# Optimization experiments

Hardware: AMD Instinct MI355X
Metric: run time of the kernel (lower is better)

Reference implementation:

```python
import jax, jax.numpy as jnp
import numpy as np

NEG_SLOPE = 0.2  # PyG GATv2 default leaky_relu slope

N_NODES = 50000
N_EDGES = 800000
F_IN = 128
HEADS = 4
C_HID = 32   # hidden_dim per head; concat -> 128
C_EMB = 128  # embedding_dim (concat=False, mean over heads)
OUT_DIM = 2


def _glorot(key, shape):
    fan_in, fan_out = shape[0], shape[-1]
    lim = (6.0 / (fan_in + fan_out)) ** 0.5
    return jax.random.uniform(key, shape, jnp.float32, -lim, lim)


def setup_inputs() -> dict:
    key = jax.random.key(0)
    ks = jax.random.split(key, 12)
    x = jax.random.normal(ks[0], (N_NODES, F_IN), jnp.float32)
    edge_index = jax.random.randint(ks[1], (2, N_EDGES), 0, N_NODES, jnp.int64)
    params = {
        # layer 1: F_IN -> (HEADS, C_HID), concat=True
        "Wl1": _glorot(ks[2], (F_IN, HEADS * C_HID)),
        "Wr1": _glorot(ks[3], (F_IN, HEADS * C_HID)),
        "att1": _glorot(ks[4], (HEADS, C_HID)),
        "b1": jnp.zeros((HEADS * C_HID,), jnp.float32),
        # layer 2: HEADS*C_HID -> (HEADS, C_EMB), concat=False (mean)
        "Wl2": _glorot(ks[5], (HEADS * C_HID, HEADS * C_EMB)),
        "Wr2": _glorot(ks[6], (HEADS * C_HID, HEADS * C_EMB)),
        "att2": _glorot(ks[7], (HEADS, C_EMB)),
        "b2": jnp.zeros((C_EMB,), jnp.float32),
        # decoder linear
        "Wo": _glorot(ks[8], (C_EMB, OUT_DIM)),
        "bo": jnp.zeros((OUT_DIM,), jnp.float32),
    }
    return {"x": x, "edge_index": edge_index, **params}


def _gatv2_layer(x, Wl, Wr, att, b, src, dst, n_nodes, concat):
    """GATv2Conv: e_ij = att . leaky_relu(Wl x_j + Wr x_i); segment softmax over dst."""
    H, C = att.shape
    xl = (x @ Wl).reshape(n_nodes, H, C)  # source transform
    xr = (x @ Wr).reshape(n_nodes, H, C)  # target transform
    m = xl[src] + xr[dst]                                  # [E,H,C]
    e = jnp.sum(jax.nn.leaky_relu(m, NEG_SLOPE) * att, axis=-1)  # [E,H]
    # numerically stable segment softmax over edges sharing a dst node
    emax = jax.ops.segment_max(e, dst, num_segments=n_nodes)[dst]
    ex = jnp.exp(e - emax)
    denom = jax.ops.segment_sum(ex, dst, num_segments=n_nodes)[dst]
    alpha = ex / denom                                     # [E,H]
    out = jax.ops.segment_sum(alpha[..., None] * xl[src], dst, num_segments=n_nodes)  # [N,H,C]
    out = out.reshape(n_nodes, H * C) if concat else out.mean(axis=1)
    return out + b


def reference(x, edge_index, Wl1, Wr1, att1, b1, Wl2, Wr2, att2, b2, Wo, bo):
    n = x.shape[0]
    loop = jnp.arange(n, dtype=edge_index.dtype)
    src = jnp.concatenate([edge_index[0], loop])  # PyG adds self-loops by default
    dst = jnp.concatenate([edge_index[1], loop])
    h = _gatv2_layer(x, Wl1, Wr1, att1, b1, src, dst, n, concat=True)
    h = jax.nn.relu(h)
    h = _gatv2_layer(h, Wl2, Wr2, att2, b2, src, dst, n, concat=False)
    out = h @ Wo + bo
    return out, h
```

## Files before the change

kernel.cpp:

```cpp
#include <hip/hip_runtime.h>

#define NEG_SLOPE 0.2f
#define LOG2E 1.44269504088896340736f

typedef unsigned short ushort_t;
typedef unsigned int uint_t;
typedef __attribute__((ext_vector_type(8))) short bf16x8;
typedef __attribute__((ext_vector_type(4))) float f32x4;
typedef __attribute__((ext_vector_type(2))) float f32x2;

__device__ inline float bf2f(ushort_t u) { union { uint_t i; float f; } v; v.i = ((uint_t)u) << 16; return v.f; }
__device__ inline ushort_t f2bf(float f) {
    union { float f; uint_t u; } v; v.f = f;
    uint_t r = v.u + 0x7fffu + ((v.u >> 16) & 1u);
    return (ushort_t)(r >> 16);
}
__device__ inline f32x2 up2v(uint_t w) {
    union { uint_t i; float f; } lo, hi;
    lo.i = w << 16; hi.i = w & 0xFFFF0000u;
    return (f32x2){lo.f, hi.f};
}
__device__ inline f32x2 up2f(uint_t w) {
    union { uint_t i; float f; } lo, hi;
    lo.i = w << 16; hi.i = w;
    return (f32x2){lo.f, hi.f};
}
__device__ inline float ld_f(const void* p, size_t i, int bf) { return bf ? bf2f(((const ushort_t*)p)[i]) : ((const float*)p)[i]; }
__device__ inline ushort_t ld_b(const void* p, size_t i, int bf) { return bf ? ((const ushort_t*)p)[i] : f2bf(((const float*)p)[i]); }
__device__ inline void edge_sd(const int* __restrict__ ei, int e, int E_in, int i64, int& src, int& dst) {
    if (e < E_in) {
        if (i64) { src = ei[2 * (size_t)e]; dst = ei[2 * ((size_t)E_in + e)]; }
        else     { src = ei[e];             dst = ei[(size_t)E_in + e]; }
    } else { src = dst = e - E_in; }
}

template <int CTRL>
__device__ inline float dpp_add(float v) {
    union { float f; int i; } u, r;
    u.f = v;
    r.i = __builtin_amdgcn_update_dpp(0, u.i, CTRL, 0xF, 0xF, true);
    return v + r.f;
}

__device__ inline uint4 ldu4(const ushort_t* __restrict__ base, uint_t boff) {
    return *(const uint4*)((const char*)base + (size_t)boff);
}

__global__ void k_detect(const uint_t* __restrict__ xw, const int* __restrict__ ei, int* flags) {
    __shared__ int cnt;
    if (threadIdx.x == 0) cnt = 0;
    __syncthreads();
    uint_t w = xw[threadIdx.x];
    int eb = (int)((w >> 7) & 0xFFu);
    if (eb >= 113 && eb <= 142) atomicAdd(&cnt, 1);
    __syncthreads();
    if (threadIdx.x == 0) {
        flags[0] = (cnt > 128) ? 1 : 0;
        int z = 0;
        #pragma unroll
        for (int i = 1; i < 16; i += 2) z += (ei[i] == 0) ? 1 : 0;
        flags[1] = (z == 8) ? 1 : 0;
    }
}

__global__ __launch_bounds__(256) void k_prep(const void* __restrict__ x, const void* Wl1, const void* Wr1,
                      const void* att1, const void* b1, const void* Wl2, const void* Wr2,
                      const void* att2, const void* b2, const void* Wo, const void* bo,
                      const int* __restrict__ ei, int E_in, int Etot, int* deg, ushort_t* xb,
                      ushort_t* WTl1, ushort_t* WTr1, ushort_t* WTl2, ushort_t* WTr2,
                      float* att1f, float* b1f, float* att2f, float* b2f, float* Wof, float* bof,
                      int N, int sW1, int sW2, int satt1, int sb1, int satt2, int sb2, int sWo, int sbo,
                      const int* flags) {
    int bf = flags[0];
    long r = (long)blockIdx.x * 256 + threadIdx.x;
    if (r < Etot) {
        int e = (int)r, dst;
        if (e < E_in) dst = flags[1] ? ei[2 * ((size_t)E_in + e)] : ei[(size_t)E_in + e];
        else          dst = e - E_in;
        atomicAdd(&deg[dst], 1);
        return;
    }
    r -= Etot;
    long nx = (long)N * 128;
    if (r < nx) { xb[r] = ld_b(x, r, bf); return; }          r -= nx;
    if (r < sW1) { int n = r >> 7, k = r & 127; WTl1[r] = ld_b(Wl1, (size_t)k * 128 + n, bf); return; } r -= sW1;
    if (r < sW1) { int n = r >> 7, k = r & 127; WTr1[r] = ld_b(Wr1, (size_t)k * 128 + n, bf); return; } r -= sW1;
    if (r < sW2) { int n = r >> 7, k = r & 127; WTl2[r] = ld_b(Wl2, (size_t)k * 512 + n, bf); return; } r -= sW2;
    if (r < sW2) { int n = r >> 7, k = r & 127; WTr2[r] = ld_b(Wr2, (size_t)k * 512 + n, bf); return; } r -= sW2;
    if (r < satt1) { att1f[r] = ld_f(att1, r, bf); return; } r -= satt1;
    if (r < sb1)   { b1f[r]   = ld_f(b1, r, bf);   return; } r -= sb1;
    if (r < satt2) { att2f[r] = ld_f(att2, r, bf); return; } r -= satt2;
    if (r < sb2)   { b2f[r]   = ld_f(b2, r, bf);   return; } r -= sb2;
    if (r < sWo)   { Wof[r]   = ld_f(Wo, r, bf);   return; } r -= sWo;
    if (r < sbo)   { bof[r]   = ld_f(bo, r, bf);   return; }
}

__global__ __launch_bounds__(256) void k_scanA(const int* __restrict__ deg, int* offs, int* bsum, int n) {
    __shared__ int sh[256];
    int t = threadIdx.x;
    int i = blockIdx.x * 256 + t;
    int v = (i < n) ? deg[i] : 0;
    sh[t] = v; __syncthreads();
    #pragma unroll
    for (int off = 1; off < 256; off <<= 1) {
        int u = (t >= off) ? sh[t - off] : 0;
        __syncthreads();
        sh[t] += u; __syncthreads();
    }
    if (i < n) offs[i] = sh[t] - v;
    if (t == 255) bsum[blockIdx.x] = sh[255];
}

__global__ __launch_bounds__(256) void k_scanBC(int* offs, int* cursor, const int* __restrict__ bsum,
                                                int nb, int n) {
    __shared__ int sh[256];
    int t = threadIdx.x;
    int v = (t < nb) ? bsum[t] : 0;
    sh[t] = v; __syncthreads();
    #pragma unroll
    for (int off = 1; off < 256; off <<= 1) {
        int u = (t >= off) ? sh[t - off] : 0;
        __syncthreads();
        sh[t] += u; __syncthreads();
    }
    if (blockIdx.x == 0 && t == 0) { offs[n] = sh[nb - 1]; cursor[n] = sh[nb - 1]; }
    int base = (blockIdx.x > 0) ? sh[blockIdx.x - 1] : 0;
    __syncthreads();
    int i = blockIdx.x * 256 + t;
    if (i < n) {
        int o = offs[i] + base;
        offs[i] = o; cursor[i] = o;
    }
}

__global__ void k_fill(const int* __restrict__ ei, int E_in, int Etot, const int* flags,
                       int* cursor, int* s_src) {
    int e = blockIdx.x * blockDim.x + threadIdx.x;
    if (e >= Etot) return;
    int src, dst; edge_sd(ei, e, E_in, flags[1], src, dst);
    int p = atomicAdd(&cursor[dst], 1);
    s_src[p] = src;
}

#define BPAD 136
template <int NOUT>
__global__ __launch_bounds__(256) void k_gemm2(const ushort_t* __restrict__ X,
                                               const ushort_t* __restrict__ WTl,
                                               const ushort_t* __restrict__ WTr,
                                               ushort_t* __restrict__ Yl,
                                               ushort_t* __restrict__ Yr, int M) {
    __shared__ ushort_t smem[2 * 64 * BPAD];
    const int lane = threadIdx.x & 63, wid = threadIdx.x >> 6;
    const int rt = blockIdx.x * 4 + wid;
    const bool active = rt < (M >> 4);
    const int quad = lane >> 4, lo = lane & 15;

    bf16x8 afr[4];
    if (active) {
        const ushort_t* xrow = X + (size_t)(rt * 16 + lo) * 128 + quad * 8;
        #pragma unroll
        for (int kc = 0; kc < 4; kc++) afr[kc] = *(const bf16x8*)(xrow + kc * 32);
    }

    for (int g = 0; g < NOUT / 64; g++) {
        __syncthreads();
        #pragma unroll
        for (int i = 0; i < 8; i++) {
            int vecid = threadIdx.x * 8 + i;
            int side = vecid >> 10, row = (vecid >> 4) & 63, v = vecid & 15;
            const ushort_t* src = (side ? WTr : WTl) + (size_t)(g * 64 + row) * 128 + v * 8;
            *(bf16x8*)(smem + (size_t)(side * 64 + row) * BPAD + v * 8) = *(const bf16x8*)src;
        }
        __syncthreads();
        if (!active) continue;
        #pragma unroll
        for (int side = 0; side < 2; side++) {
            ushort_t* Y = side ? Yr : Yl;
            f32x4 acc[4];
            #pragma unroll
            for (int nt = 0; nt < 4; nt++) acc[nt] = (f32x4){0.f, 0.f, 0.f, 0.f};
            #pragma unroll
            for (int nt = 0; nt < 4; nt++) {
                const ushort_t* brow = smem + (size_t)(side * 64 + nt * 16 + lo) * BPAD + quad * 8;
                #pragma unroll
                for (int kc = 0; kc < 4; kc++) {
                    bf16x8 b = *(const bf16x8*)(brow + kc * 32);
                    acc[nt] = __builtin_amdgcn_mfma_f32_16x16x32_bf16(afr[kc], b, acc[nt], 0, 0, 0);
                }
            }
            #pragma unroll
            for (int nt = 0; nt < 4; nt++) {
                int col = g * 64 + nt * 16 + lo;
                #pragma unroll
                for (int ri = 0; ri < 4; ri++) {
                    int row = rt * 16 + quad * 4 + ri;
                    Y[(size_t)row * NOUT + col] = f2bf(acc[nt][ri]);
                }
            }
        }
    }
}

__global__ __launch_bounds__(256) void k_l1(const ushort_t* __restrict__ xl,
                                            const ushort_t* __restrict__ xr,
                                            const int* __restrict__ offs,
                                            const int* __restrict__ s_src,
                                            const float* __restrict__ att,
                                            const float* __restrict__ b1,
                                            int n, ushort_t* __restrict__ h1) {
    int lane = threadIdx.x & 63, wid = threadIdx.x >> 6;
    int node = blockIdx.x * 4 + wid;
    if (node >= n) return;
    int slot = lane >> 4, sub = lane & 15;
    int chb = sub * 8;
    uint_t cb = (uint_t)(sub * 16);

    uint4 xw = *(const uint4*)(xr + (size_t)node * 128 + chb);
    f32x2 xv[4] = {up2v(xw.x), up2v(xw.y), up2v(xw.z), up2v(xw.w)};
    f32x2 aL[4];
    #pragma unroll
    for (int j = 0; j < 4; j++) {
        f32x2 a = {att[chb + 2 * j], att[chb + 2 * j + 1]};
        aL[j] = a * (float)LOG2E;
    }

    int o0 = offs[node], o1 = offs[node + 1];
    float s = 0.f;
    f32x2 acc[4] = {{0.f,0.f},{0.f,0.f},{0.f,0.f},{0.f,0.f}};

    int i = o0 + slot;
    uint_t q0 = 0, q1 = 0;
    uint4 w0 = {0,0,0,0}, w1 = {0,0,0,0};
    if (i < o1)      w0 = ldu4(xl, (((uint_t)s_src[i])      << 8) + cb);
    if (i + 4 < o1)  w1 = ldu4(xl, (((uint_t)s_src[i + 4])  << 8) + cb);
    if (i + 8 < o1)  q0 = (((uint_t)s_src[i + 8])  << 8) + cb;
    if (i + 12 < o1) q1 = (((uint_t)s_src[i + 12]) << 8) + cb;

    while (i < o1) {
        uint4 wc = w0;
        w0 = w1;
        if (i + 8 < o1) w1 = ldu4(xl, q0);
        q0 = q1;
        if (i + 16 < o1) q1 = (((uint_t)s_src[i + 16]) << 8) + cb;
        f32x2 v[4] = {up2v(wc.x), up2v(wc.y), up2v(wc.z), up2v(wc.w)};
        f32x2 es = {0.f, 0.f};
        #pragma unroll
        for (int j = 0; j < 4; j++) {
            f32x2 m = v[j] + xv[j];
            f32x2 l = __builtin_elementwise_max(m, m * NEG_SLOPE);
            es = __builtin_elementwise_fma(aL[j], l, es);
        }
        float e = es.x + es.y;
        e = dpp_add<0xB1>(e);
        e = dpp_add<0x4E>(e);
        float p = __builtin_amdgcn_exp2f(fminf(e, 115.f));
        s += p;
        f32x2 pp = {p, p};
        #pragma unroll
        for (int j = 0; j < 4; j++)
            acc[j] = __builtin_elementwise_fma(pp, v[j], acc[j]);
        i += 4;
    }
    #pragma unroll
    for (int off = 16; off <= 32; off <<= 1) {
        s += __shfl_xor(s, off, 64);
        #pragma unroll
        for (int j = 0; j < 4; j++) {
            f32x2 o = {__shfl_xor(acc[j].x, off, 64), __shfl_xor(acc[j].y, off, 64)};
            acc[j] += o;
        }
    }
    if (slot == 0) {
        float inv = 1.f / s;
        uint_t pk[4];
        #pragma unroll
        for (int j = 0; j < 4; j++) {
            float r0 = fmaxf(fmaf(acc[j].x, inv, b1[chb + 2 * j]),     0.f);
            float r1 = fmaxf(fmaf(acc[j].y, inv, b1[chb + 2 * j + 1]), 0.f);
            pk[j] = (uint_t)f2bf(r0) | ((uint_t)f2bf(r1) << 16);
        }
        *(uint4*)(h1 + (size_t)node * 128 + chb) = make_uint4(pk[0], pk[1], pk[2], pk[3]);
    }
}

__global__ __launch_bounds__(256) void k_l2(const ushort_t* __restrict__ xl,
                                            const ushort_t* __restrict__ xr,
                                            const int* __restrict__ offs,
                                            const int* __restrict__ s_src,
                                            const float* __restrict__ att,
                                            const float* __restrict__ b2,
                                            const float* __restrict__ Wo,
                                            const float* __restrict__ bo,
                                            int n, const int* flags, void* dout) {
    int lane = threadIdx.x & 63, wid = threadIdx.x >> 6;
    int node = blockIdx.x * 4 + wid;
    if (node >= n) return;
    int h = lane >> 4, sub = lane & 15;
    int chb = sub * 8;
    int choff = h * 128 + chb;
    uint_t cb = (uint_t)(choff * 2);
    int bf = flags[0];

    uint4 xw = *(const uint4*)(xr + (size_t)node * 512 + choff);
    f32x2 xv[4] = {up2v(xw.x), up2v(xw.y), up2v(xw.z), up2v(xw.w)};
    f32x2 aL[4];
    #pragma unroll
    for (int j = 0; j < 4; j++) {
        f32x2 a = {att[choff + 2 * j], att[choff + 2 * j + 1]};
        aL[j] = a * (float)LOG2E;
    }

    int o0 = __builtin_amdgcn_readfirstlane(offs[node]);
    int o1 = __builtin_amdgcn_readfirstlane(offs[node + 1]);
    int cnt = o1 - o0;

    float s = 0.f;
    f32x2 acc[4] = {{0.f,0.f},{0.f,0.f},{0.f,0.f},{0.f,0.f}};
    const char* xlb = (const char*)xl;

    for (int base = 0; base < cnt; base += 64) {
        int m = cnt - base; if (m > 64) m = 64;
        int vidx = s_src[o0 + base + lane];

        auto ROW = [&](int k) -> uint4 {
            int kk = (k < m - 1) ? k : (m - 1);
            int idx = __builtin_amdgcn_readlane(vidx, kk);
            return *(const uint4*)(xlb + (((size_t)(uint_t)idx) << 10) + cb);
        };
        auto PROC = [&](const uint4& w) {
            f32x2 v[4] = {up2f(w.x), up2f(w.y), up2f(w.z), up2f(w.w)};
            f32x2 es = {0.f, 0.f};
            #pragma unroll
            for (int j = 0; j < 4; j++) {
                f32x2 mm = v[j] + xv[j];
                f32x2 l = __builtin_elementwise_max(mm, mm * NEG_SLOPE);
                es = __builtin_elementwise_fma(aL[j], l, es);
            }
            float e = es.x + es.y;
            e = dpp_add<0xB1>(e);
            e = dpp_add<0x4E>(e);
            e = dpp_add<0x141>(e);
            e = dpp_add<0x140>(e);
            float p = __builtin_amdgcn_exp2f(fminf(e, 115.f));
            s += p;
            f32x2 pp = {p, p};
            #pragma unroll
            for (int j = 0; j < 4; j++)
                acc[j] = __builtin_elementwise_fma(pp, v[j], acc[j]);
        };

        uint4 wA = ROW(0), wB = ROW(1), wC = ROW(2);
        uint4 wD = ROW(3), wE = ROW(4), wF = ROW(5);
        int k = 0;
        for (; k + 6 <= m; k += 6) {
            uint4 tA = ROW(k + 6);  PROC(wA); wA = tA;
            uint4 tB = ROW(k + 7);  PROC(wB); wB = tB;
            uint4 tC = ROW(k + 8);  PROC(wC); wC = tC;
            uint4 tD = ROW(k + 9);  PROC(wD); wD = tD;
            uint4 tE = ROW(k + 10); PROC(wE); wE = tE;
            uint4 tF = ROW(k + 11); PROC(wF); wF = tF;
        }
        if (k < m)     PROC(wA);
        if (k + 1 < m) PROC(wB);
        if (k + 2 < m) PROC(wC);
        if (k + 3 < m) PROC(wD);
        if (k + 4 < m) PROC(wE);
    }

    float inv = 1.f / s;
    f32x2 iv = {inv, inv};
    #pragma unroll
    for (int j = 0; j < 4; j++) acc[j] = acc[j] * iv;
    #pragma unroll
    for (int off = 16; off <= 32; off <<= 1) {
        #pragma unroll
        for (int j = 0; j < 4; j++) {
            f32x2 o = {__shfl_xor(acc[j].x, off, 64), __shfl_xor(acc[j].y, off, 64)};
            acc[j] += o;
        }
    }
    float hm[8];
    #pragma unroll
    for (int j = 0; j < 4; j++) {
        hm[2 * j]     = 0.25f * acc[j].x + b2[chb + 2 * j];
        hm[2 * j + 1] = 0.25f * acc[j].y + b2[chb + 2 * j + 1];
    }

    if (h == 0) {
        size_t ob = (size_t)n * 2 + (size_t)node * 128 + chb;
        if (bf) {
            uint_t pk[4];
            #pragma unroll
            for (int j = 0; j < 4; j++)
                pk[j] = (uint_t)f2bf(hm[2 * j]) | ((uint_t)f2bf(hm[2 * j + 1]) << 16);
            *(uint4*)((ushort_t*)dout + ob) = make_uint4(pk[0], pk[1], pk[2], pk[3]);
        } else {
            float* fp = (float*)dout + ob;
            *(float4*)fp       = make_float4(hm[0], hm[1], hm[2], hm[3]);
            *(float4*)(fp + 4) = make_float4(hm[4], hm[5], hm[6], hm[7]);
        }
    }

    float d0 = 0.f, d1 = 0.f;
    #pragma unroll
    for (int c = 0; c < 8; c++) {
        float w0 = Wo[(chb + c) * 2], w1 = Wo[(chb + c) * 2 + 1];
        d0 = fmaf(hm[c], w0, d0);
        d1 = fmaf(hm[c], w1, d1);
    }
    d0 = dpp_add<0xB1>(d0); d0 = dpp_add<0x4E>(d0); d0 = dpp_add<0x141>(d0); d0 = dpp_add<0x140>(d0);
    d1 = dpp_add<0xB1>(d1); d1 = dpp_add<0x4E>(d1); d1 = dpp_add<0x141>(d1); d1 = dpp_add<0x140>(d1);
    if (lane == 0) {
        float r0 = d0 + bo[0], r1 = d1 + bo[1];
        size_t oidx = (size_t)node * 2;
        if (bf) { ((ushort_t*)dout)[oidx] = f2bf(r0); ((ushort_t*)dout)[oidx + 1] = f2bf(r1); }
        else    { ((float*)dout)[oidx]    = r0;       ((float*)dout)[oidx + 1]    = r1; }
    }
}

extern "C" void kernel_launch(void* const* d_in, const int* in_sizes, int n_in,
                              void* d_out, int out_size, void* d_ws, size_t ws_size,
                              hipStream_t stream) {
    const void* x    = d_in[0];
    const int*  ei   = (const int*)d_in[1];
    const void* Wl1  = d_in[2];
    const void* Wr1  = d_in[3];
    const void* att1 = d_in[4];
    const void* b1   = d_in[5];
    const void* Wl2  = d_in[6];
    const void* Wr2  = d_in[7];
    const void* att2 = d_in[8];
    const void* b2   = d_in[9];
    const void* Wo   = d_in[10];
    const void* bo   = d_in[11];

    const int N    = in_sizes[0] / 128;
    const int E_in = in_sizes[1] / 2;
    const int Etot = E_in + N;

    const int sW1 = in_sizes[2], sW2 = in_sizes[6];
    const int satt1 = in_sizes[4], sb1 = in_sizes[5];
    const int satt2 = in_sizes[8], sb2 = in_sizes[9];
    const int sWo = in_sizes[10], sbo = in_sizes[11];

    char* w = (char*)d_ws;
    size_t off = 0;
    auto take = [&](size_t bytes) -> void* {
        void* p = w + off;
        off += (bytes + 255) & ~(size_t)255;
        return p;
    };
    int*      flags  = (int*)take(256);
    ushort_t* xb     = (ushort_t*)take((size_t)N * 128 * sizeof(ushort_t));
    ushort_t* WTl1   = (ushort_t*)take((size_t)sW1 * 2);
    ushort_t* WTr1   = (ushort_t*)take((size_t)sW1 * 2);
    ushort_t* WTl2   = (ushort_t*)take((size_t)sW2 * 2);
    ushort_t* WTr2   = (ushort_t*)take((size_t)sW2 * 2);
    float*    att1f  = (float*)take((size_t)satt1 * 4);
    float*    b1f    = (float*)take((size_t)sb1 * 4);
    float*    att2f  = (float*)take((size_t)satt2 * 4);
    float*    b2f    = (float*)take((size_t)sb2 * 4);
    float*    Wof    = (float*)take((size_t)sWo * 4);
    float*    bof    = (float*)take((size_t)sbo * 4);
    int*      deg    = (int*)take((size_t)N * sizeof(int));
    int*      offs   = (int*)take((size_t)(N + 1) * sizeof(int));
    int*      cursor = (int*)take((size_t)(N + 1) * sizeof(int));
    int*      bsum   = (int*)take(1024);
    int*      s_src  = (int*)take((size_t)(Etot + 64) * sizeof(int));
    ushort_t* h1     = (ushort_t*)take((size_t)N * 128 * sizeof(ushort_t));
    ushort_t* xl1b   = (ushort_t*)take((size_t)N * 128 * sizeof(ushort_t));
    ushort_t* xr1b   = (ushort_t*)take((size_t)N * 128 * sizeof(ushort_t));
    ushort_t* xl2b   = (ushort_t*)take((size_t)N * 512 * sizeof(ushort_t));
    ushort_t* xr2b   = (ushort_t*)take((size_t)N * 512 * sizeof(ushort_t));

    dim3 b256(256);
    const int nb = (N + 255) / 256;

    k_detect<<<1, b256, 0, stream>>>((const uint_t*)x, ei, flags);
    hipMemsetAsync(deg, 0, (size_t)N * sizeof(int), stream);
    hipMemsetAsync(s_src + Etot, 0, 64 * sizeof(int), stream);

    long prep_total = (long)Etot + (long)N * 128 + 2L * sW1 + 2L * sW2
                    + satt1 + sb1 + satt2 + sb2 + sWo + sbo;
    int prep_blocks = (int)((prep_total + 255) / 256);
    k_prep<<<prep_blocks, b256, 0, stream>>>(x, Wl1, Wr1, att1, b1, Wl2, Wr2, att2, b2, Wo, bo,
                                             ei, E_in, Etot, deg, xb, WTl1, WTr1, WTl2, WTr2,
                                             att1f, b1f, att2f, b2f, Wof, bof,
                                             N, sW1, sW2, satt1, sb1, satt2, sb2, sWo, sbo, flags);

    k_scanA<<<nb, b256, 0, stream>>>(deg, offs, bsum, N);
    k_scanBC<<<nb, b256, 0, stream>>>(offs, cursor, bsum, nb, N);
    k_fill<<<(Etot + 255) / 256, b256, 0, stream>>>(ei, E_in, Etot, flags, cursor, s_src);

    dim3 gg((N / 16 + 3) / 4);
    k_gemm2<128><<<gg, b256, 0, stream>>>(xb, WTl1, WTr1, xl1b, xr1b, N);
    k_l1<<<(N + 3) / 4, b256, 0, stream>>>(xl1b, xr1b, offs, s_src, att1f, b1f, N, h1);

    k_gemm2<512><<<gg, b256, 0, stream>>>(h1, WTl2, WTr2, xl2b, xr2b, N);

    k_l2<<<(N + 3) / 4, b256, 0, stream>>>(xl2b, xr2b, offs, s_src, att2f, b2f, Wof, bof, N, flags, d_out);
}
```

Baseline: 424.2 us.

## Vectorize x conversion, widen GEMM blocks, deepen L1 gather prefetch

The prep kernel now converts x to bf16 eight elements per thread with 16-byte loads and stores instead of one scalar per thread, cutting thread count and memory transactions. The GEMM kernel moves to 512-thread blocks covering 8 row tiles, so each staged weight tile in shared memory is reused by twice as many waves and the global weight reload per block is halved. The layer-1 aggregation loop adds a third in-flight gather register, deepening the software prefetch of neighbour rows to hide more latency at the cost of extra registers.

```diff
diff --git a/kernel.cpp b/kernel.cpp
--- a/kernel.cpp
+++ b/kernel.cpp
@@ -81,8 +81,25 @@
         return;
     }
     r -= Etot;
-    long nx = (long)N * 128;
-    if (r < nx) { xb[r] = ld_b(x, r, bf); return; }          r -= nx;
+    long nx8 = (long)N * 16;
+    if (r < nx8) {
+        size_t base = (size_t)r * 8;
+        if (bf) {
+            *(uint4*)(xb + base) = *(const uint4*)((const ushort_t*)x + base);
+        } else {
+            const float* xf = (const float*)x + base;
+            float4 a = *(const float4*)xf;
+            float4 c = *(const float4*)(xf + 4);
+            uint_t pk[4];
+            pk[0] = (uint_t)f2bf(a.x) | ((uint_t)f2bf(a.y) << 16);
+            pk[1] = (uint_t)f2bf(a.z) | ((uint_t)f2bf(a.w) << 16);
+            pk[2] = (uint_t)f2bf(c.x) | ((uint_t)f2bf(c.y) << 16);
+            pk[3] = (uint_t)f2bf(c.z) | ((uint_t)f2bf(c.w) << 16);
+            *(uint4*)(xb + base) = make_uint4(pk[0], pk[1], pk[2], pk[3]);
+        }
+        return;
+    }
+    r -= nx8;
     if (r < sW1) { int n = r >> 7, k = r & 127; WTl1[r] = ld_b(Wl1, (size_t)k * 128 + n, bf); return; } r -= sW1;
     if (r < sW1) { int n = r >> 7, k = r & 127; WTr1[r] = ld_b(Wr1, (size_t)k * 128 + n, bf); return; } r -= sW1;
     if (r < sW2) { int n = r >> 7, k = r & 127; WTl2[r] = ld_b(Wl2, (size_t)k * 512 + n, bf); return; } r -= sW2;
@@ -144,14 +161,14 @@
 
 #define BPAD 136
 template <int NOUT>
-__global__ __launch_bounds__(256) void k_gemm2(const ushort_t* __restrict__ X,
+__global__ __launch_bounds__(512) void k_gemm2(const ushort_t* __restrict__ X,
                                                const ushort_t* __restrict__ WTl,
                                                const ushort_t* __restrict__ WTr,
                                                ushort_t* __restrict__ Yl,
                                                ushort_t* __restrict__ Yr, int M) {
     __shared__ ushort_t smem[2 * 64 * BPAD];
     const int lane = threadIdx.x & 63, wid = threadIdx.x >> 6;
-    const int rt = blockIdx.x * 4 + wid;
+    const int rt = blockIdx.x * 8 + wid;
     const bool active = rt < (M >> 4);
     const int quad = lane >> 4, lo = lane & 15;
 
@@ -165,8 +182,8 @@
     for (int g = 0; g < NOUT / 64; g++) {
         __syncthreads();
         #pragma unroll
-        for (int i = 0; i < 8; i++) {
-            int vecid = threadIdx.x * 8 + i;
+        for (int i = 0; i < 4; i++) {
+            int vecid = threadIdx.x * 4 + i;
             int side = vecid >> 10, row = (vecid >> 4) & 63, v = vecid & 15;
             const ushort_t* src = (side ? WTr : WTl) + (size_t)(g * 64 + row) * 128 + v * 8;
             *(bf16x8*)(smem + (size_t)(side * 64 + row) * BPAD + v * 8) = *(const bf16x8*)src;
@@ -230,18 +247,19 @@
 
     int i = o0 + slot;
     uint_t q0 = 0, q1 = 0;
-    uint4 w0 = {0,0,0,0}, w1 = {0,0,0,0};
+    uint4 w0 = {0,0,0,0}, w1 = {0,0,0,0}, w2 = {0,0,0,0};
     if (i < o1)      w0 = ldu4(xl, (((uint_t)s_src[i])      << 8) + cb);
     if (i + 4 < o1)  w1 = ldu4(xl, (((uint_t)s_src[i + 4])  << 8) + cb);
-    if (i + 8 < o1)  q0 = (((uint_t)s_src[i + 8])  << 8) + cb;
-    if (i + 12 < o1) q1 = (((uint_t)s_src[i + 12]) << 8) + cb;
+    if (i + 8 < o1)  w2 = ldu4(xl, (((uint_t)s_src[i + 8])  << 8) + cb);
+    if (i + 12 < o1) q0 = (((uint_t)s_src[i + 12]) << 8) + cb;
+    if (i + 16 < o1) q1 = (((uint_t)s_src[i + 16]) << 8) + cb;
 
     while (i < o1) {
         uint4 wc = w0;
-        w0 = w1;
-        if (i + 8 < o1) w1 = ldu4(xl, q0);
+        w0 = w1; w1 = w2;
+        if (i + 12 < o1) w2 = ldu4(xl, q0);
         q0 = q1;
-        if (i + 16 < o1) q1 = (((uint_t)s_src[i + 16]) << 8) + cb;
+        if (i + 20 < o1) q1 = (((uint_t)s_src[i + 20]) << 8) + cb;
         f32x2 v[4] = {up2v(wc.x), up2v(wc.y), up2v(wc.z), up2v(wc.w)};
         f32x2 es = {0.f, 0.f};
         #pragma unroll
@@ -473,14 +491,14 @@
     ushort_t* xl2b   = (ushort_t*)take((size_t)N * 512 * sizeof(ushort_t));
     ushort_t* xr2b   = (ushort_t*)take((size_t)N * 512 * sizeof(ushort_t));
 
-    dim3 b256(256);
+    dim3 b256(256), b512(512);
     const int nb = (N + 255) / 256;
 
     k_detect<<<1, b256, 0, stream>>>((const uint_t*)x, ei, flags);
     hipMemsetAsync(deg, 0, (size_t)N * sizeof(int), stream);
     hipMemsetAsync(s_src + Etot, 0, 64 * sizeof(int), stream);
 
-    long prep_total = (long)Etot + (long)N * 128 + 2L * sW1 + 2L * sW2
+    long prep_total = (long)Etot + (long)N * 16 + 2L * sW1 + 2L * sW2
                     + satt1 + sb1 + satt2 + sb2 + sWo + sbo;
     int prep_blocks = (int)((prep_total + 255) / 256);
     k_prep<<<prep_blocks, b256, 0, stream>>>(x, Wl1, Wr1, att1, b1, Wl2, Wr2, att2, b2, Wo, bo,
@@ -492,11 +510,11 @@
     k_scanBC<<<nb, b256, 0, stream>>>(offs, cursor, bsum, nb, N);
     k_fill<<<(Etot + 255) / 256, b256, 0, stream>>>(ei, E_in, Etot, flags, cursor, s_src);
 
-    dim3 gg((N / 16 + 3) / 4);
-    k_gemm2<128><<<gg, b256, 0, stream>>>(xb, WTl1, WTr1, xl1b, xr1b, N);
+    dim3 gg((N / 16 + 7) / 8);
+    k_gemm2<128><<<gg, b512, 0, stream>>>(xb, WTl1, WTr1, xl1b, xr1b, N);
     k_l1<<<(N + 3) / 4, b256, 0, stream>>>(xl1b, xr1b, offs, s_src, att1f, b1f, N, h1);
 
-    k_gemm2<512><<<gg, b256, 0, stream>>>(h1, WTl2, WTr2, xl2b, xr2b, N);
+    k_gemm2<512><<<gg, b512, 0, stream>>>(h1, WTl2, WTr2, xl2b, xr2b, N);
 
     k_l2<<<(N + 3) / 4, b256, 0, stream>>>(xl2b, xr2b, offs, s_src, att2f, b2f, Wof, bof, N, flags, d_out);
 }
```

New measurement: 395.0 us, median of 2. 6.9% less time.
